# Performance work log

Hardware: AMD Instinct MI355X
Metric: run time of the kernel (lower is better)

Reference implementation:

```python
import jax, jax.numpy as jnp
import numpy as np

# Static config (must match init_kwargs)
IMG_H, IMG_W = 48, 160
BEV_H, BEV_W = 128, 128
X_MIN, X_MAX, Y_MIN, Y_MAX = -51.2, 51.2, -51.2, 51.2
RES_X = (X_MAX - X_MIN) / BEV_W
RES_Y = (Y_MAX - Y_MIN) / BEV_H
C, D, B = 128, 64, 2


def setup_inputs() -> dict:
    key = jax.random.key(0)
    k1, k2, k3, k4 = jax.random.split(key, 4)
    img_features = jax.random.normal(k1, (B, C, IMG_H, IMG_W), dtype=jnp.float32)
    # depth distribution per pixel (softmax over D, as a depth net would emit)
    depth_probs = jax.nn.softmax(jax.random.normal(k2, (B, D, IMG_H, IMG_W), dtype=jnp.float32), axis=1)
    # depth bin centers: 1m .. 60m
    depth_values = jnp.linspace(1.0, 60.0, D, dtype=jnp.float32)
    # realistic pinhole intrinsics (feature-map scale) with tiny per-cam jitter
    fx, fy, cx, cy = 120.0, 120.0, IMG_W / 2.0, IMG_H / 2.0
    K0 = jnp.array([[fx, 0.0, cx], [0.0, fy, cy], [0.0, 0.0, 1.0]], dtype=jnp.float32)
    K = K0[None] + 0.01 * jax.random.normal(k3, (B, 3, 3), dtype=jnp.float32) * jnp.array(
        [[1.0, 0.0, 1.0], [0.0, 1.0, 1.0], [0.0, 0.0, 0.0]], dtype=jnp.float32)
    # cam->lidar extrinsic: cam z (forward) -> lidar x, cam x -> -lidar y, cam y -> -lidar z
    R0 = jnp.array([[0.0, 0.0, 1.0], [-1.0, 0.0, 0.0], [0.0, -1.0, 0.0]], dtype=jnp.float32)
    t0 = jnp.array([1.5, 0.0, 1.8], dtype=jnp.float32)
    T0 = jnp.eye(4, dtype=jnp.float32).at[:3, :3].set(R0).at[:3, 3].set(t0)
    T = T0[None] + jnp.zeros((B, 4, 4), dtype=jnp.float32)
    T = T.at[:, :3, 3].add(0.05 * jax.random.normal(k4, (B, 3), dtype=jnp.float32))
    return {"img_features": img_features, "depth_probs": depth_probs,
            "depth_values": depth_values, "K": K, "T": T}


def _lss_forward(img_features, depth_probs, depth_values, K, T):
    Bn, Cn, H, W = img_features.shape
    Dn = depth_values.shape[0]
    # homogeneous pixel grid [H, W, 3]
    gx, gy = jnp.meshgrid(jnp.arange(W, dtype=jnp.float32),
                          jnp.arange(H, dtype=jnp.float32), indexing="xy")
    grid = jnp.stack([gx, gy, jnp.ones_like(gx)], axis=-1)
    # unproject: rays [B, H, W, 3]
    K_inv = jnp.linalg.inv(K)
    rays = jnp.einsum("bij,hwj->bhwi", K_inv, grid)
    # points in camera frame [B, D, H, W, 3]
    pts_cam = depth_values[None, :, None, None, None] * rays[:, None]
    # camera -> lidar
    pts = jnp.einsum("bij,bdhwj->bdhwi", T[:, :3, :3], pts_cam) + T[:, None, None, None, :3, 3]
    x, y, z = pts[..., 0], pts[..., 1], pts[..., 2]
    # torch .long() truncates toward zero -> astype int32 matches
    bx = ((x - X_MIN) / RES_X).astype(jnp.int32)
    by = ((y - Y_MIN) / RES_Y).astype(jnp.int32)
    valid = (bx >= 0) & (bx < BEV_W) & (by >= 0) & (by < BEV_H) & (z > 0)
    # depth-weighted features [B, D, H, W, C], masked instead of gathered
    weighted = jnp.einsum("bchw,bdhw->bdhwc", img_features, depth_probs)
    weighted = weighted * valid[..., None]
    idx = jnp.where(valid, by * BEV_W + bx, 0).reshape(Bn, -1)
    feats = weighted.reshape(Bn, -1, Cn)
    bev_flat = jax.vmap(lambda f, i: jax.ops.segment_sum(f, i, num_segments=BEV_H * BEV_W))(feats, idx)
    return bev_flat.reshape(Bn, BEV_H, BEV_W, Cn).transpose(0, 3, 1, 2)


def reference(img_features, depth_probs, depth_values, K, T):
    return _lss_forward(img_features, depth_probs, depth_values, K, T)
```

## Files before the change

### kernel.cpp

```cpp
#include <hip/hip_runtime.h>

constexpr int IMG_H = 48, IMG_W = 160;
constexpr int HW    = IMG_H * IMG_W;
constexpr int BEV_H = 128, BEV_W = 128;
constexpr int NCELL = BEV_H * BEV_W;
constexpr int C_DIM = 128, D_DIM = 64, B_DIM = 2;
constexpr int NCELL_TOT = B_DIM * NCELL;
constexpr int NPIX_TOT  = B_DIM * HW;
constexpr int NPTS      = NPIX_TOT * D_DIM;
constexpr int MAX_ENTRIES = NPTS;
constexpr int BIGCHUNK = 256;
constexpr int WAVES_PER_BLK = 4;
constexpr int NSHARD = 16;
constexpr int CNT_BLOCKS = NPTS / 256;
constexpr int TRN_BLOCKS = (HW / 32) * (C_DIM / 32) * B_DIM;
constexpr int PREP_TOTAL = CNT_BLOCKS + TRN_BLOCKS;
constexpr int SCAN_BLOCKS = NCELL_TOT / 256;
constexpr int GATHER_BLOCKS = NPTS / (BIGCHUNK * WAVES_PER_BLK);
constexpr float X_MIN = -51.2f, Y_MIN = -51.2f;
constexpr float RES_X = 102.4f / 128.0f;
constexpr float RES_Y = 102.4f / 128.0f;

typedef _Float16 half2v __attribute__((ext_vector_type(2)));

constexpr size_t WS_IMG_T = 0;
constexpr size_t WS_TOT   = WS_IMG_T + (size_t)B_DIM * HW * C_DIM / 2;
constexpr size_t WS_HIST2 = WS_TOT + 4;
constexpr size_t WS_OUT_T = WS_HIST2 + (size_t)NSHARD * NCELL_TOT;
constexpr size_t WS_OFFS  = WS_OUT_T + (size_t)NCELL_TOT * C_DIM;
constexpr size_t WS_EKEY  = WS_OFFS + NCELL_TOT + 4;
constexpr size_t WS_EW16  = WS_EKEY + MAX_ENTRIES;
constexpr size_t MEMSET_WORDS = 4 + (size_t)NSHARD * NCELL_TOT;
constexpr int OUT_T_F4 = NCELL_TOT * C_DIM / 4;

__device__ inline int point_shard(int tid) {
    return ((tid >> 2) + (tid >> 8)) & (NSHARD - 1);
}

__device__ inline void make_ray(const float* __restrict__ K, int b, float gx, float gy,
                                float& rx, float& ry, float& rz) {
    const float* Kb = K + b * 9;
    const float a00 = Kb[0], a01 = Kb[1], a02 = Kb[2];
    const float a10 = Kb[3], a11 = Kb[4], a12 = Kb[5];
    const float a20 = Kb[6], a21 = Kb[7], a22 = Kb[8];
    const float det = a00 * (a11 * a22 - a12 * a21)
                    - a01 * (a10 * a22 - a12 * a20)
                    + a02 * (a10 * a21 - a11 * a20);
    const float inv = 1.0f / det;
    const float i00 =  (a11 * a22 - a12 * a21) * inv;
    const float i01 = -(a01 * a22 - a02 * a21) * inv;
    const float i02 =  (a01 * a12 - a02 * a11) * inv;
    const float i10 = -(a10 * a22 - a12 * a20) * inv;
    const float i11 =  (a00 * a22 - a02 * a20) * inv;
    const float i12 = -(a00 * a12 - a02 * a10) * inv;
    const float i20 =  (a10 * a21 - a11 * a20) * inv;
    const float i21 = -(a00 * a21 - a01 * a20) * inv;
    const float i22 =  (a00 * a11 - a01 * a10) * inv;
    rx = i00 * gx + i01 * gy + i02;
    ry = i10 * gx + i11 * gy + i12;
    rz = i20 * gx + i21 * gy + i22;
}

__device__ inline int point_gcell(int tid, const float* __restrict__ dv,
                                  const float* __restrict__ K,
                                  const float* __restrict__ T) {
    const int pix = tid % HW;
    const int bd  = tid / HW;
    const int d   = bd % D_DIM;
    const int b   = bd / D_DIM;
    const int h = pix / IMG_W, w = pix % IMG_W;
    float rx, ry, rz;
    make_ray(K, b, (float)w, (float)h, rx, ry, rz);
    const float* Tb = T + b * 16;
    const float dep = dv[d];
    const float px = dep * rx, py = dep * ry, pz = dep * rz;
    const float x = Tb[0] * px + Tb[1] * py + Tb[2]  * pz + Tb[3];
    const float y = Tb[4] * px + Tb[5] * py + Tb[6]  * pz + Tb[7];
    const float z = Tb[8] * px + Tb[9] * py + Tb[10] * pz + Tb[11];
    const int bx = (int)((x - X_MIN) / RES_X);
    const int by = (int)((y - Y_MIN) / RES_Y);
    const bool valid = (bx >= 0) && (bx < BEV_W) && (by >= 0) && (by < BEV_H) && (z > 0.0f);
    return valid ? (b * NCELL + by * BEV_W + bx) : -1;
}

__device__ inline bool wave_runs(int gcell, int lane, int& run_len, int& leader_idx) {
    const int left = __shfl_up(gcell, 1);
    const bool is_leader = (lane == 0) || (left != gcell);
    const unsigned long long lmask = __ballot(is_leader);
    const unsigned long long rest = (lane == 63) ? 0ULL : (lmask >> (lane + 1));
    const int f = __ffsll((unsigned long long)rest);
    run_len = f ? f : (64 - lane);
    const unsigned long long below =
        lmask & ((lane == 63) ? ~0ULL : ((1ULL << (lane + 1)) - 1ULL));
    leader_idx = 63 - __clzll((long long)below);
    return is_leader;
}

__global__ __launch_bounds__(256) void k_prep(const float* __restrict__ img,
                                              _Float16* __restrict__ img_t,
                                              const float* __restrict__ dv,
                                              const float* __restrict__ K,
                                              const float* __restrict__ T,
                                              int* __restrict__ hist2,
                                              float4* __restrict__ out_t4) {
    __shared__ float tile[32][33];
    const int t = threadIdx.x;

    {
        const int i = blockIdx.x * 256 + t;
        if (i < OUT_T_F4) out_t4[i] = make_float4(0.f, 0.f, 0.f, 0.f);
    }

    if (blockIdx.x < CNT_BLOCKS) {
        const int tid = blockIdx.x * 256 + t;
        const int gcell = point_gcell(tid, dv, K, T);
        const int lane = t & 63;
        int run_len, leader_idx;
        const bool lead = wave_runs(gcell, lane, run_len, leader_idx);
        if (lead && gcell >= 0)
            atomicAdd(&hist2[(size_t)point_shard(tid) * NCELL_TOT + gcell], run_len);
    } else {
        const int bi = blockIdx.x - CNT_BLOCKS;
        const int px_t = bi % (HW / 32);
        const int c_t  = (bi / (HW / 32)) % (C_DIM / 32);
        const int b    = bi / ((HW / 32) * (C_DIM / 32));
        const int tx = t & 31, ty = t >> 5;
        const int pix0 = px_t * 32, c0 = c_t * 32;
        #pragma unroll
        for (int j = 0; j < 32; j += 8)
            tile[ty + j][tx] = img[((size_t)(b * C_DIM + c0 + ty + j)) * HW + pix0 + tx];
        __syncthreads();
        #pragma unroll
        for (int j = 0; j < 32; j += 8)
            img_t[((size_t)(b * HW + pix0 + ty + j)) * C_DIM + c0 + tx] =
                (_Float16)tile[tx][ty + j];
    }
}

__global__ __launch_bounds__(256) void k_scan(int* __restrict__ hist2,
                                              int* __restrict__ offs,
                                              int* __restrict__ tot) {
    __shared__ int lds[256];
    __shared__ int s_base;
    const int b = blockIdx.x;
    const int t = threadIdx.x;
    const int cell = b * 256 + t;
    int run = 0;
    #pragma unroll
    for (int sh = 0; sh < NSHARD; ++sh) {
        const size_t idx = (size_t)sh * NCELL_TOT + cell;
        const int c = hist2[idx];
        hist2[idx] = run;
        run += c;
    }
    const int h = run;
    lds[t] = h;
    __syncthreads();
    #pragma unroll
    for (int off = 1; off < 256; off <<= 1) {
        const int v = (t >= off) ? lds[t - off] : 0;
        __syncthreads();
        lds[t] += v;
        __syncthreads();
    }
    const int incl = lds[t];
    const int S = lds[255];
    if (t == 0) {
        s_base = atomicAdd(&tot[0], S);
        const int arr = atomicAdd(&tot[1], 1);
        if (arr == SCAN_BLOCKS - 1)
            offs[NCELL_TOT] = atomicAdd(&tot[0], 0);
    }
    __syncthreads();
    offs[cell] = s_base + incl - h;
}

__global__ __launch_bounds__(256) void k_fill(const float* __restrict__ dp,
                                              const float* __restrict__ dv,
                                              const float* __restrict__ K,
                                              const float* __restrict__ T,
                                              const int* __restrict__ offs,
                                              int* __restrict__ cursor2,
                                              int* __restrict__ ekey,
                                              unsigned short* __restrict__ ew16) {
    const int tid = blockIdx.x * 256 + threadIdx.x;
    const int gcell = point_gcell(tid, dv, K, T);
    const int lane = threadIdx.x & 63;
    int run_len, leader_idx;
    const bool lead = wave_runs(gcell, lane, run_len, leader_idx);
    int base = 0;
    if (lead && gcell >= 0)
        base = offs[gcell]
             + atomicAdd(&cursor2[(size_t)point_shard(tid) * NCELL_TOT + gcell], run_len);
    base = __shfl(base, leader_idx);
    if (gcell < 0) return;
    const int slot = base + (lane - leader_idx);
    const float p = dp[tid];
    ekey[slot] = (gcell << 13) | (tid % HW);
    ew16[slot] = (unsigned short)__float2uint_rn(p * 65535.0f);
}

__global__ __launch_bounds__(256) void k_chunk_gather(
    const _Float16* __restrict__ img_t,
    const int* __restrict__ offs,
    const int* __restrict__ ekey,
    const unsigned short* __restrict__ ew16,
    float* __restrict__ out_t)
{
    const int total = offs[NCELL_TOT];
    const int wave  = threadIdx.x >> 6;
    const int lane  = threadIdx.x & 63;
    const int ci    = blockIdx.x * WAVES_PER_BLK + wave;
    const int nch   = (total + BIGCHUNK - 1) / BIGCHUNK;
    if (ci >= nch) return;
    const int base  = ci * BIGCHUNK;
    const int c2    = lane * 2;

    int mykey0, mykey1, mykey2, mykey3;
    int mywi0, mywi1, mywi2, mywi3;
#define LOADKEYS(S, KV, WV)                                                      \
    do {                                                                         \
        const int idx = base + (S) * 64 + lane;                                  \
        const int eidx = min(idx, total - 1);                                    \
        KV = ekey[eidx];                                                         \
        const float w = (idx < total) ? (float)ew16[eidx] * (1.0f / 65535.0f)    \
                                      : 0.0f;                                    \
        WV = __float_as_int(w);                                                  \
    } while (0)
    LOADKEYS(0, mykey0, mywi0);
    LOADKEYS(1, mykey1, mywi1);
    LOADKEYS(2, mykey2, mywi2);
    LOADKEYS(3, mykey3, mywi3);
#undef LOADKEYS

    const int fc    = __builtin_amdgcn_readlane(mykey0, 0) >> 13;
    const int lcell = __builtin_amdgcn_readlane(mykey3, 63) >> 13;
    const bool shared_first = (base > 0) && ((ekey[base - 1] >> 13) == fc);
    const bool shared_last  = (base + BIGCHUNK < total) &&
                              ((ekey[base + BIGCHUNK] >> 13) == lcell);

    int prev = fc;
    float2 acc = make_float2(0.0f, 0.0f);

#define LOAD16(KV, g, V)                                                         \
    do {                                                                         \
        _Pragma("unroll")                                                        \
        for (int k = 0; k < 16; ++k) {                                           \
            const int key = __builtin_amdgcn_readlane(KV, (g) * 16 + k);         \
            const int pix = key & 8191;                                          \
            const int bb  = key >> 27;                                           \
            V[k] = *reinterpret_cast<const half2v*>(                             \
                &img_t[((size_t)(bb * HW + pix)) * C_DIM + c2]);                 \
        }                                                                        \
    } while (0)

#define FLUSHP(cell)                                                             \
    do {                                                                         \
        float* o = &out_t[(size_t)(cell) * C_DIM + c2];                          \
        const bool shared_ = ((cell) == fc && shared_first) ||                   \
                             ((cell) == lcell && shared_last);                   \
        if (shared_) {                                                           \
            atomicAdd(o, acc.x);                                                 \
            atomicAdd(o + 1, acc.y);                                             \
        } else {                                                                 \
            *reinterpret_cast<float2*>(o) = acc;            \
        }                                                                        \
    } while (0)

#define ACC16(KV, WV, g, V)                                                      \
    do {                                                                         \
        _Pragma("unroll")                                                        \
        for (int k = 0; k < 16; ++k) {                                           \
            const int   key = __builtin_amdgcn_readlane(KV, (g) * 16 + k);       \
            const float wgt =                                                    \
                __int_as_float(__builtin_amdgcn_readlane(WV, (g) * 16 + k));     \
            const int gcell = key >> 13;                                         \
            if (gcell != prev) {                              \
                FLUSHP(prev);                                                    \
                acc = make_float2(0.0f, 0.0f);                                   \
                prev = gcell;                                                    \
            }                                                                    \
            acc.x = fmaf((float)V[k][0], wgt, acc.x);                            \
            acc.y = fmaf((float)V[k][1], wgt, acc.y);                            \
        }                                                                        \
    } while (0)

#define SUB64(KV, WV)                                                            \
    do {                                                                         \
        half2v v0[16], v1[16], v2[16], v3[16];                                   \
        LOAD16(KV, 0, v0);                                                       \
        LOAD16(KV, 1, v1);                                                       \
        LOAD16(KV, 2, v2);                                                       \
        LOAD16(KV, 3, v3);                                                       \
        ACC16(KV, WV, 0, v0);                                                    \
        ACC16(KV, WV, 1, v1);                                                    \
        ACC16(KV, WV, 2, v2);                                                    \
        ACC16(KV, WV, 3, v3);                                                    \
    } while (0)

    SUB64(mykey0, mywi0);
    SUB64(mykey1, mywi1);
    SUB64(mykey2, mywi2);
    SUB64(mykey3, mywi3);
    FLUSHP(prev);

#undef LOAD16
#undef FLUSHP
#undef ACC16
#undef SUB64
}

__global__ __launch_bounds__(256) void k_untranspose(const float* __restrict__ out_t,
                                                     float* __restrict__ out) {
    __shared__ float tile[32][33];
    const int b = blockIdx.z;
    const int tx = threadIdx.x, ty = threadIdx.y;
    const int cell0 = blockIdx.x * 32, c0 = blockIdx.y * 32;
    const float* src = out_t + (size_t)b * NCELL * C_DIM;
    #pragma unroll
    for (int j = 0; j < 32; j += 8)
        tile[ty + j][tx] = src[((size_t)(cell0 + ty + j)) * C_DIM + c0 + tx];
    __syncthreads();
    #pragma unroll
    for (int j = 0; j < 32; j += 8)
        out[((size_t)(b * C_DIM + c0 + ty + j)) * NCELL + cell0 + tx] = tile[tx][ty + j];
}

extern "C" void kernel_launch(void* const* d_in, const int* in_sizes, int n_in,
                              void* d_out, int out_size, void* d_ws, size_t ws_size,
                              hipStream_t stream) {
    const float* img = (const float*)d_in[0];
    const float* dp  = (const float*)d_in[1];
    const float* dv  = (const float*)d_in[2];
    const float* K   = (const float*)d_in[3];
    const float* T   = (const float*)d_in[4];
    float* out = (float*)d_out;

    _Float16* img_t = (_Float16*)d_ws;
    int*   tot    = (int*)d_ws + WS_TOT;
    int*   hist2  = (int*)d_ws + WS_HIST2;
    float* out_t  = (float*)d_ws + WS_OUT_T;
    int*   offs   = (int*)d_ws + WS_OFFS;
    int*   ekey   = (int*)d_ws + WS_EKEY;
    unsigned short* ew16 = (unsigned short*)((int*)d_ws + WS_EW16);
    (void)ws_size;

    hipMemsetAsync(tot, 0, MEMSET_WORDS * sizeof(int), stream);

    k_prep<<<PREP_TOTAL, 256, 0, stream>>>(img, img_t, dv, K, T, hist2,
                                           (float4*)out_t);
    k_scan<<<SCAN_BLOCKS, 256, 0, stream>>>(hist2, offs, tot);
    k_fill<<<NPTS / 256, 256, 0, stream>>>(dp, dv, K, T, offs, hist2, ekey, ew16);
    k_chunk_gather<<<GATHER_BLOCKS, 256, 0, stream>>>(img_t, offs, ekey, ew16, out_t);
    k_untranspose<<<dim3(NCELL / 32, C_DIM / 32, B_DIM), dim3(32, 8), 0, stream>>>(
        out_t, out);
}
```

Measured before the change: 143.5 us.

## Split wave into two half-waves processing separate chunk halves with 8-byte loads

The gather kernel now splits each 64-lane wave into two 32-lane halves. Each half processes one 128-entry half of the chunk and loads four fp16 channels per lane instead of two. Loads are software-pipelined across groups with double buffers, replacing the earlier load-all-then-accumulate pattern. This cuts the serial per-entry loop iterations in half and widens memory accesses, at the cost of divergent flush handling, extra readlanes and an additional shared boundary between the two halves that needs atomics.

```diff
diff --git a/kernel.cpp b/kernel.cpp
--- a/kernel.cpp
+++ b/kernel.cpp
@@ -21,7 +21,7 @@
 constexpr float RES_X = 102.4f / 128.0f;
 constexpr float RES_Y = 102.4f / 128.0f;
 
-typedef _Float16 half2v __attribute__((ext_vector_type(2)));
+typedef _Float16 half4v __attribute__((ext_vector_type(4)));
 
 constexpr size_t WS_IMG_T = 0;
 constexpr size_t WS_TOT   = WS_IMG_T + (size_t)B_DIM * HW * C_DIM / 2;
@@ -214,7 +214,8 @@
     const int nch   = (total + BIGCHUNK - 1) / BIGCHUNK;
     if (ci >= nch) return;
     const int base  = ci * BIGCHUNK;
-    const int c2    = lane * 2;
+    const bool hlo  = lane < 32;
+    const int sl4   = (lane & 31) * 4;
 
     int mykey0, mykey1, mykey2, mykey3;
     int mywi0, mywi1, mywi2, mywi3;
@@ -233,81 +234,99 @@
     LOADKEYS(3, mykey3, mywi3);
 #undef LOADKEYS
 
-    const int fc    = __builtin_amdgcn_readlane(mykey0, 0) >> 13;
-    const int lcell = __builtin_amdgcn_readlane(mykey3, 63) >> 13;
-    const bool shared_first = (base > 0) && ((ekey[base - 1] >> 13) == fc);
-    const bool shared_last  = (base + BIGCHUNK < total) &&
-                              ((ekey[base + BIGCHUNK] >> 13) == lcell);
-
-    int prev = fc;
-    float2 acc = make_float2(0.0f, 0.0f);
-
-#define LOAD16(KV, g, V)                                                         \
+    const int fcA = __builtin_amdgcn_readlane(mykey0, 0) >> 13;
+    const int lcA = __builtin_amdgcn_readlane(mykey1, 63) >> 13;
+    const int fcB = __builtin_amdgcn_readlane(mykey2, 0) >> 13;
+    const int lcB = __builtin_amdgcn_readlane(mykey3, 63) >> 13;
+    const bool sfA = (base > 0) && ((ekey[base - 1] >> 13) == fcA);
+    const bool slA = (lcA == fcB);
+    const bool sfB = slA;
+    const bool slB = (base + BIGCHUNK < total) &&
+                     ((ekey[base + BIGCHUNK] >> 13) == lcB);
+
+    int prevA = fcA, prevB = fcB;
+    float4 acc = make_float4(0.0f, 0.0f, 0.0f, 0.0f);
+
+#define FLUSH2(cdA, cdB)                                                         \
+    do {                                                                         \
+        const bool myc = hlo ? (cdA) : (cdB);                                    \
+        if (myc) {                                                               \
+            const int pc = hlo ? prevA : prevB;                                  \
+            const bool sh = hlo                                                  \
+                ? ((pc == fcA && sfA) || (pc == lcA && slA))                     \
+                : ((pc == fcB && sfB) || (pc == lcB && slB));                    \
+            float* o = &out_t[(size_t)pc * C_DIM + sl4];                         \
+            if (sh) {                                                            \
+                atomicAdd(o, acc.x);                                             \
+                atomicAdd(o + 1, acc.y);                                         \
+                atomicAdd(o + 2, acc.z);                                         \
+                atomicAdd(o + 3, acc.w);                                         \
+            } else {                                                             \
+                *reinterpret_cast<float4*>(o) = acc;        \
+            }                                                                    \
+            acc = make_float4(0.0f, 0.0f, 0.0f, 0.0f);                           \
+        }                                                                        \
+    } while (0)
+
+#define LOADG(gg, KA, KB, V)                                                     \
     do {                                                                         \
         _Pragma("unroll")                                                        \
         for (int k = 0; k < 16; ++k) {                                           \
-            const int key = __builtin_amdgcn_readlane(KV, (g) * 16 + k);         \
-            const int pix = key & 8191;                                          \
-            const int bb  = key >> 27;                                           \
-            V[k] = *reinterpret_cast<const half2v*>(                             \
-                &img_t[((size_t)(bb * HW + pix)) * C_DIM + c2]);                 \
+            const int ln = ((gg) & 3) * 16 + k;                                  \
+            const int kA = __builtin_amdgcn_readlane(KA, ln);                    \
+            const int kB = __builtin_amdgcn_readlane(KB, ln);                    \
+            const int rA = (kA & 8191) + (kA >> 27) * HW;                        \
+            const int rB = (kB & 8191) + (kB >> 27) * HW;                        \
+            const int row = hlo ? rA : rB;                                       \
+            V[k] = *reinterpret_cast<const half4v*>(                             \
+                &img_t[(size_t)row * C_DIM + sl4]);                              \
         }                                                                        \
     } while (0)
 
-#define FLUSHP(cell)                                                             \
-    do {                                                                         \
-        float* o = &out_t[(size_t)(cell) * C_DIM + c2];                          \
-        const bool shared_ = ((cell) == fc && shared_first) ||                   \
-                             ((cell) == lcell && shared_last);                   \
-        if (shared_) {                                                           \
-            atomicAdd(o, acc.x);                                                 \
-            atomicAdd(o + 1, acc.y);                                             \
-        } else {                                                                 \
-            *reinterpret_cast<float2*>(o) = acc;            \
-        }                                                                        \
-    } while (0)
-
-#define ACC16(KV, WV, g, V)                                                      \
+#define ACCG(gg, KA, KB, WA, WB, V)                                              \
     do {                                                                         \
         _Pragma("unroll")                                                        \
         for (int k = 0; k < 16; ++k) {                                           \
-            const int   key = __builtin_amdgcn_readlane(KV, (g) * 16 + k);       \
-            const float wgt =                                                    \
-                __int_as_float(__builtin_amdgcn_readlane(WV, (g) * 16 + k));     \
-            const int gcell = key >> 13;                                         \
-            if (gcell != prev) {                              \
-                FLUSHP(prev);                                                    \
-                acc = make_float2(0.0f, 0.0f);                                   \
-                prev = gcell;                                                    \
+            const int ln = ((gg) & 3) * 16 + k;                                  \
+            const int kA = __builtin_amdgcn_readlane(KA, ln);                    \
+            const int kB = __builtin_amdgcn_readlane(KB, ln);                    \
+            const float w = hlo                                                  \
+                ? __int_as_float(__builtin_amdgcn_readlane(WA, ln))              \
+                : __int_as_float(__builtin_amdgcn_readlane(WB, ln));             \
+            const int cA = kA >> 13, cB = kB >> 13;                              \
+            if (cA != prevA || cB != prevB) {                                    \
+                FLUSH2(cA != prevA, cB != prevB);                                \
+                prevA = cA; prevB = cB;                                          \
             }                                                                    \
-            acc.x = fmaf((float)V[k][0], wgt, acc.x);                            \
-            acc.y = fmaf((float)V[k][1], wgt, acc.y);                            \
+            acc.x = fmaf((float)V[k][0], w, acc.x);                              \
+            acc.y = fmaf((float)V[k][1], w, acc.y);                              \
+            acc.z = fmaf((float)V[k][2], w, acc.z);                              \
+            acc.w = fmaf((float)V[k][3], w, acc.w);                              \
         }                                                                        \
     } while (0)
 
-#define SUB64(KV, WV)                                                            \
-    do {                                                                         \
-        half2v v0[16], v1[16], v2[16], v3[16];                                   \
-        LOAD16(KV, 0, v0);                                                       \
-        LOAD16(KV, 1, v1);                                                       \
-        LOAD16(KV, 2, v2);                                                       \
-        LOAD16(KV, 3, v3);                                                       \
-        ACC16(KV, WV, 0, v0);                                                    \
-        ACC16(KV, WV, 1, v1);                                                    \
-        ACC16(KV, WV, 2, v2);                                                    \
-        ACC16(KV, WV, 3, v3);                                                    \
-    } while (0)
-
-    SUB64(mykey0, mywi0);
-    SUB64(mykey1, mywi1);
-    SUB64(mykey2, mywi2);
-    SUB64(mykey3, mywi3);
-    FLUSHP(prev);
-
-#undef LOAD16
-#undef FLUSHP
-#undef ACC16
-#undef SUB64
+    half4v va[16], vb[16];
+    LOADG(0, mykey0, mykey2, va);
+    LOADG(1, mykey0, mykey2, vb);
+    ACCG(0, mykey0, mykey2, mywi0, mywi2, va);
+    LOADG(2, mykey0, mykey2, va);
+    ACCG(1, mykey0, mykey2, mywi0, mywi2, vb);
+    LOADG(3, mykey0, mykey2, vb);
+    ACCG(2, mykey0, mykey2, mywi0, mywi2, va);
+    LOADG(4, mykey1, mykey3, va);
+    ACCG(3, mykey0, mykey2, mywi0, mywi2, vb);
+    LOADG(5, mykey1, mykey3, vb);
+    ACCG(4, mykey1, mykey3, mywi1, mywi3, va);
+    LOADG(6, mykey1, mykey3, va);
+    ACCG(5, mykey1, mykey3, mywi1, mywi3, vb);
+    LOADG(7, mykey1, mykey3, vb);
+    ACCG(6, mykey1, mykey3, mywi1, mywi3, va);
+    ACCG(7, mykey1, mykey3, mywi1, mywi3, vb);
+    FLUSH2(true, true);
+
+#undef LOADG
+#undef FLUSH2
+#undef ACCG
 }
 
 __global__ __launch_bounds__(256) void k_untranspose(const float* __restrict__ out_t,
```

Result: slower. 166.7 us (+16.2%).
